# Kernel tuning notes

Measured on AMD Instinct MI355X. Metric: run time of the kernel, lower is better.

## Reference

```python
import jax, jax.numpy as jnp
import numpy as np

DIM = 32  # fixed internal node dim
N_GRAPHS = 64


def setup_inputs() -> dict:
    key = jax.random.key(0)
    ks = jax.random.split(key, 16)
    N, E, F_N, F_E, H = 12500, 200000, 16, 8, 32
    inp = {
        "x": jax.random.normal(ks[0], (N, F_N), dtype=jnp.float32),
        "edge_index": jax.random.randint(ks[1], (2, E), 0, N, dtype=jnp.int64),
        "edge_attr": jax.random.normal(ks[2], (E, F_E), dtype=jnp.float32),
        "batch": jnp.sort(jax.random.randint(ks[3], (N,), 0, N_GRAPHS, dtype=jnp.int64)),
        "lin0_w": jax.random.normal(ks[4], (DIM, F_N), dtype=jnp.float32) * 0.1,
        "lin0_b": jax.random.normal(ks[5], (DIM,), dtype=jnp.float32) * 0.1,
        "nn_w": jax.random.normal(ks[6], (DIM * H, F_E), dtype=jnp.float32) * 0.1,
        "nn_b": jax.random.normal(ks[7], (DIM * H,), dtype=jnp.float32) * 0.1,
        "root_w": jax.random.normal(ks[8], (DIM, H), dtype=jnp.float32) * 0.1,
        "conv_b": jax.random.normal(ks[9], (H,), dtype=jnp.float32) * 0.1,
        "lin1_w": jax.random.normal(ks[10], (16, H), dtype=jnp.float32) * 0.1,
        "lin1_b": jax.random.normal(ks[11], (16,), dtype=jnp.float32) * 0.1,
        "lin2_w": jax.random.normal(ks[12], (1, 16), dtype=jnp.float32) * 0.1,
        "lin2_b": jax.random.normal(ks[13], (1,), dtype=jnp.float32) * 0.1,
    }
    return inp


def reference(x, edge_index, edge_attr, batch, lin0_w, lin0_b, nn_w, nn_b,
              root_w, conv_b, lin1_w, lin1_b, lin2_w, lin2_b):
    N = x.shape[0]
    H = conv_b.shape[0]
    # lin0 + relu -> node features [N, DIM]
    out = jax.nn.relu(x @ lin0_w.T + lin0_b)
    # NNConv: per-edge weight matrices from edge MLP (single Linear)
    src, dst = edge_index[0], edge_index[1]
    w_e = (edge_attr @ nn_w.T + nn_b).reshape(-1, DIM, H)  # [E, DIM, H]
    msg = jnp.einsum('ed,edh->eh', out[src], w_e)          # gather + per-edge matmul
    agg = jax.ops.segment_sum(msg, dst, num_segments=N)     # scatter-add
    h = jax.nn.relu(agg + out @ root_w + conv_b)             # root weight + bias
    # global add pool over graphs
    u = jax.ops.segment_sum(h, batch, num_segments=N_GRAPHS)  # [G, H]
    o = jax.nn.relu(u @ lin1_w.T + lin1_b)
    o = o @ lin2_w.T + lin2_b
    return o.reshape(-1)
```

## Files before the change

kernel.cpp:

```cpp
#include <hip/hip_runtime.h>

#define DIMN 32
#define HD   32
#define FN   16
#define FE   8
#define NG   64
#define NPB1 16
#define NPB3 64

__global__ __launch_bounds__(256) void k1_node_pre(
    const float* __restrict__ x, const float* __restrict__ lin0_w,
    const float* __restrict__ lin0_b, const float* __restrict__ nn_w,
    const float* __restrict__ nn_b,
    float* __restrict__ outn, float* __restrict__ G, float* __restrict__ bmsg,
    float* __restrict__ agg, float* __restrict__ u, int N)
{
    __shared__ float s_nnw[DIMN * HD * FE];
    __shared__ float s_nnb[DIMN * HD];
    __shared__ float s_l0w[DIMN * FN];
    __shared__ float s_l0b[DIMN];
    __shared__ float s_out[NPB1 * DIMN];

    const int tid = threadIdx.x;
    for (int i = tid; i < DIMN * HD * FE; i += 256) s_nnw[i] = nn_w[i];
    for (int i = tid; i < DIMN * HD; i += 256)      s_nnb[i] = nn_b[i];
    for (int i = tid; i < DIMN * FN; i += 256)      s_l0w[i] = lin0_w[i];
    if (tid < DIMN) s_l0b[tid] = lin0_b[tid];

    const int n0 = blockIdx.x * NPB1;

    {
        const int a0 = n0 * HD;
        const int a1 = min((n0 + NPB1) * HD, N * HD);
        for (int i = a0 + tid; i < a1; i += 256) agg[i] = 0.f;
        if (blockIdx.x < (NG * HD) / 256) u[blockIdx.x * 256 + tid] = 0.f;
    }
    __syncthreads();

    #pragma unroll
    for (int pass = 0; pass < 2; ++pass) {
        const int nl = pass * 8 + (tid >> 5);
        const int d  = tid & 31;
        const int n  = n0 + nl;
        if (n < N) {
            float s = s_l0b[d];
            const float* xr = x + (size_t)n * FN;
            #pragma unroll
            for (int j = 0; j < FN; ++j) s = fmaf(xr[j], s_l0w[d * FN + j], s);
            s = fmaxf(s, 0.f);
            s_out[nl * DIMN + d] = s;
            outn[(size_t)n * DIMN + d] = s;
        }
    }
    __syncthreads();

    for (int nl = 0; nl < NPB1; ++nl) {
        const int n = n0 + nl;
        if (n >= N) break;
        float g = 0.f;
        #pragma unroll 8
        for (int d = 0; d < DIMN; ++d)
            g = fmaf(s_out[nl * DIMN + d], s_nnw[d * 256 + tid], g);
        G[(size_t)n * 256 + tid] = g;
    }

    #pragma unroll
    for (int pass = 0; pass < 2; ++pass) {
        const int nl = pass * 8 + (tid >> 5);
        const int h  = tid & 31;
        const int n  = n0 + nl;
        if (n < N) {
            float b = 0.f;
            #pragma unroll 8
            for (int d = 0; d < DIMN; ++d)
                b = fmaf(s_out[nl * DIMN + d], s_nnb[d * HD + h], b);
            bmsg[(size_t)n * HD + h] = b;
        }
    }
}

__global__ __launch_bounds__(256) void k2_edge(
    const int* __restrict__ ei, const float* __restrict__ ea,
    const float* __restrict__ G, const float* __restrict__ bmsg,
    float* __restrict__ agg, int E)
{
    const int t = blockIdx.x * 256 + threadIdx.x;
    const int e = t >> 5;
    const int h = t & 31;
    if (e >= E) return;

    const int src = ei[e];
    const int dst = ei[E + e];

    const float* gp = G + (size_t)src * 256 + h * 8;
    const float4 ga = *(const float4*)(gp);
    const float4 gb = *(const float4*)(gp + 4);
    const float4 e0 = *(const float4*)(ea + (size_t)e * 8);
    const float4 e1 = *(const float4*)(ea + (size_t)e * 8 + 4);

    float acc = bmsg[(size_t)src * HD + h];
    acc = fmaf(e0.x, ga.x, acc);
    acc = fmaf(e0.y, ga.y, acc);
    acc = fmaf(e0.z, ga.z, acc);
    acc = fmaf(e0.w, ga.w, acc);
    acc = fmaf(e1.x, gb.x, acc);
    acc = fmaf(e1.y, gb.y, acc);
    acc = fmaf(e1.z, gb.z, acc);
    acc = fmaf(e1.w, gb.w, acc);

    atomicAdd(agg + (size_t)dst * HD + h, acc);
}

__global__ __launch_bounds__(256) void k3_node_upd(
    const float* __restrict__ agg, const float* __restrict__ outn,
    const float* __restrict__ root_w, const float* __restrict__ conv_b,
    const int* __restrict__ batch, float* __restrict__ u, int N)
{
    __shared__ float s_rw[DIMN * HD];
    __shared__ float s_cb[HD];
    const int tid = threadIdx.x;
    for (int i = tid; i < DIMN * HD; i += 256) s_rw[i] = root_w[i];
    if (tid < HD) s_cb[tid] = conv_b[tid];
    __syncthreads();

    const int sg   = tid >> 5;
    const int h    = tid & 31;
    const int base = blockIdx.x * NPB3 + sg * (NPB3 / 8);

    float acc  = 0.f;
    int  g_cur = -1;
    #pragma unroll
    for (int i = 0; i < NPB3 / 8; ++i) {
        const int n = base + i;
        if (n >= N) break;

        float v = agg[(size_t)n * HD + h] + s_cb[h];
        const float* orow = outn + (size_t)n * DIMN;
        #pragma unroll 8
        for (int k = 0; k < DIMN; ++k)
            v = fmaf(orow[k], s_rw[k * HD + h], v);
        v = fmaxf(v, 0.f);

        const int g = (int)batch[n];
        if (g != g_cur) {
            if (g_cur >= 0) atomicAdd(u + (size_t)g_cur * HD + h, acc);
            g_cur = g;
            acc = v;
        } else {
            acc += v;
        }
    }
    if (g_cur >= 0) atomicAdd(u + (size_t)g_cur * HD + h, acc);
}

__global__ __launch_bounds__(64) void k4_head(
    const float* __restrict__ u, const float* __restrict__ lin1_w,
    const float* __restrict__ lin1_b, const float* __restrict__ lin2_w,
    const float* __restrict__ lin2_b, float* __restrict__ outp)
{
    const int g = threadIdx.x;
    if (g >= NG) return;

    float ur[HD];
    #pragma unroll
    for (int hh = 0; hh < HD; ++hh) ur[hh] = u[(size_t)g * HD + hh];

    float acc = lin2_b[0];
    #pragma unroll
    for (int i = 0; i < 16; ++i) {
        float o = lin1_b[i];
        #pragma unroll
        for (int hh = 0; hh < HD; ++hh)
            o = fmaf(ur[hh], lin1_w[i * HD + hh], o);
        o = fmaxf(o, 0.f);
        acc = fmaf(o, lin2_w[i], acc);
    }
    outp[g] = acc;
}

extern "C" void kernel_launch(void* const* d_in, const int* in_sizes, int n_in,
                              void* d_out, int out_size, void* d_ws, size_t ws_size,
                              hipStream_t stream)
{
    const float* x      = (const float*)d_in[0];
    const int*   ei     = (const int*)  d_in[1];
    const float* ea     = (const float*)d_in[2];
    const int*   batch  = (const int*)  d_in[3];
    const float* lin0_w = (const float*)d_in[4];
    const float* lin0_b = (const float*)d_in[5];
    const float* nn_w   = (const float*)d_in[6];
    const float* nn_b   = (const float*)d_in[7];
    const float* root_w = (const float*)d_in[8];
    const float* conv_b = (const float*)d_in[9];
    const float* lin1_w = (const float*)d_in[10];
    const float* lin1_b = (const float*)d_in[11];
    const float* lin2_w = (const float*)d_in[12];
    const float* lin2_b = (const float*)d_in[13];

    const int N = in_sizes[0] / FN;
    const int E = in_sizes[2] / FE;

    float* ws   = (float*)d_ws;
    float* outn = ws;
    float* G    = outn + (size_t)N * DIMN;
    float* bmsg = G    + (size_t)N * 256;
    float* agg  = bmsg + (size_t)N * DIMN;
    float* u    = agg  + (size_t)N * DIMN;

    const int nb1 = (N + NPB1 - 1) / NPB1;
    k1_node_pre<<<nb1, 256, 0, stream>>>(x, lin0_w, lin0_b, nn_w, nn_b,
                                         outn, G, bmsg, agg, u, N);

    const int nb2 = (E * 32 + 255) / 256;
    k2_edge<<<nb2, 256, 0, stream>>>(ei, ea, G, bmsg, agg, E);

    const int nb3 = (N + NPB3 - 1) / NPB3;
    k3_node_upd<<<nb3, 256, 0, stream>>>(agg, outn, root_w, conv_b, batch, u, N);

    k4_head<<<1, 64, 0, stream>>>(u, lin1_w, lin1_b, lin2_w, lin2_b, (float*)d_out);
}
```

Measured before the change: 157.9 us.

## Bucket edges by destination and gather messages per node instead of scatter atomics

Replaces the per-edge scatter kernel, which issued 32 float atomicAdds per edge into agg, with a bucketing pass. That pass does one integer atomic per edge to build fixed-capacity per-destination edge lists, with a slow per-edge fallback for nodes that overflow. A fused gather kernel then has one wavefront per group of nodes sum its incoming messages in registers, apply the root weight with shuffles, and pool into graphs. This removes most float atomic traffic and the separate node-update kernel, at the cost of an extra eidx buffer, an unsorted gather, and load imbalance on high-degree nodes.

Result: slower. 175.9 us (+11.4%).

```diff
diff --git a/kernel.cpp b/kernel.cpp
--- a/kernel.cpp
+++ b/kernel.cpp
@@ -6,14 +6,15 @@
 #define FE   8
 #define NG   64
 #define NPB1 16
-#define NPB3 64
+#define CAP  64
+#define NPW  4
 
 __global__ __launch_bounds__(256) void k1_node_pre(
     const float* __restrict__ x, const float* __restrict__ lin0_w,
     const float* __restrict__ lin0_b, const float* __restrict__ nn_w,
     const float* __restrict__ nn_b,
     float* __restrict__ outn, float* __restrict__ G, float* __restrict__ bmsg,
-    float* __restrict__ agg, float* __restrict__ u, int N)
+    float* __restrict__ agg, float* __restrict__ u, int* __restrict__ deg, int N)
 {
     __shared__ float s_nnw[DIMN * HD * FE];
     __shared__ float s_nnb[DIMN * HD];
@@ -33,6 +34,7 @@
         const int a0 = n0 * HD;
         const int a1 = min((n0 + NPB1) * HD, N * HD);
         for (int i = a0 + tid; i < a1; i += 256) agg[i] = 0.f;
+        if (tid < NPB1 && n0 + tid < N) deg[n0 + tid] = 0;
         if (blockIdx.x < (NG * HD) / 256) u[blockIdx.x * 256 + tid] = 0.f;
     }
     __syncthreads();
@@ -79,39 +81,33 @@
     }
 }
 
-__global__ __launch_bounds__(256) void k2_edge(
+__global__ __launch_bounds__(256) void kb_bucket(
     const int* __restrict__ ei, const float* __restrict__ ea,
     const float* __restrict__ G, const float* __restrict__ bmsg,
-    float* __restrict__ agg, int E)
-{
-    const int t = blockIdx.x * 256 + threadIdx.x;
-    const int e = t >> 5;
-    const int h = t & 31;
+    int* __restrict__ deg, int* __restrict__ eidx, float* __restrict__ agg, int E)
+{
+    const int e = blockIdx.x * 256 + threadIdx.x;
     if (e >= E) return;
-
-    const int src = ei[e];
     const int dst = ei[E + e];
-
-    const float* gp = G + (size_t)src * 256 + h * 8;
-    const float4 ga = *(const float4*)(gp);
-    const float4 gb = *(const float4*)(gp + 4);
-    const float4 e0 = *(const float4*)(ea + (size_t)e * 8);
-    const float4 e1 = *(const float4*)(ea + (size_t)e * 8 + 4);
-
-    float acc = bmsg[(size_t)src * HD + h];
-    acc = fmaf(e0.x, ga.x, acc);
-    acc = fmaf(e0.y, ga.y, acc);
-    acc = fmaf(e0.z, ga.z, acc);
-    acc = fmaf(e0.w, ga.w, acc);
-    acc = fmaf(e1.x, gb.x, acc);
-    acc = fmaf(e1.y, gb.y, acc);
-    acc = fmaf(e1.z, gb.z, acc);
-    acc = fmaf(e1.w, gb.w, acc);
-
-    atomicAdd(agg + (size_t)dst * HD + h, acc);
-}
-
-__global__ __launch_bounds__(256) void k3_node_upd(
+    const int pos = atomicAdd(&deg[dst], 1);
+    if (pos < CAP) {
+        eidx[dst * CAP + pos] = e;
+    } else {
+        const int src = ei[e];
+        for (int h = 0; h < HD; ++h) {
+            float m = bmsg[(size_t)src * HD + h];
+            #pragma unroll
+            for (int f = 0; f < FE; ++f)
+                m = fmaf(ea[(size_t)e * FE + f], G[(size_t)src * 256 + h * FE + f], m);
+            atomicAdd(agg + (size_t)dst * HD + h, m);
+        }
+    }
+}
+
+__global__ __launch_bounds__(256) void k23_gather_upd(
+    const int* __restrict__ ei, const float* __restrict__ ea,
+    const float* __restrict__ G, const float* __restrict__ bmsg,
+    const int* __restrict__ deg, const int* __restrict__ eidx,
     const float* __restrict__ agg, const float* __restrict__ outn,
     const float* __restrict__ root_w, const float* __restrict__ conv_b,
     const int* __restrict__ batch, float* __restrict__ u, int N)
@@ -123,34 +119,61 @@
     if (tid < HD) s_cb[tid] = conv_b[tid];
     __syncthreads();
 
-    const int sg   = tid >> 5;
-    const int h    = tid & 31;
-    const int base = blockIdx.x * NPB3 + sg * (NPB3 / 8);
-
-    float acc  = 0.f;
-    int  g_cur = -1;
-    #pragma unroll
-    for (int i = 0; i < NPB3 / 8; ++i) {
-        const int n = base + i;
+    const int lane  = tid & 63;
+    const int h     = lane & 31;
+    const int p     = lane >> 5;
+    const int wid   = (blockIdx.x * 256 + tid) >> 6;
+    const int nbase = wid * NPW;
+
+    float accp  = 0.f;
+    int   g_cur = -1;
+
+    for (int i = 0; i < NPW; ++i) {
+        const int n = nbase + i;
         if (n >= N) break;
 
-        float v = agg[(size_t)n * HD + h] + s_cb[h];
-        const float* orow = outn + (size_t)n * DIMN;
-        #pragma unroll 8
+        const int dn = min(deg[n], CAP);
+        float acc = 0.f;
+        for (int j = p; j < dn; j += 2) {
+            const int e   = eidx[n * CAP + j];
+            const int src = ei[e];
+            const float4 w0 = *(const float4*)(ea + (size_t)e * FE);
+            const float4 w1 = *(const float4*)(ea + (size_t)e * FE + 4);
+            const float* gp = G + (size_t)src * 256 + h * 8;
+            const float4 ga = *(const float4*)(gp);
+            const float4 gb = *(const float4*)(gp + 4);
+            float m = bmsg[(size_t)src * HD + h];
+            m = fmaf(w0.x, ga.x, m);
+            m = fmaf(w0.y, ga.y, m);
+            m = fmaf(w0.z, ga.z, m);
+            m = fmaf(w0.w, ga.w, m);
+            m = fmaf(w1.x, gb.x, m);
+            m = fmaf(w1.y, gb.y, m);
+            m = fmaf(w1.z, gb.z, m);
+            m = fmaf(w1.w, gb.w, m);
+            acc += m;
+        }
+        acc += __shfl_xor(acc, 32);
+
+        float v = acc + s_cb[h] + agg[(size_t)n * HD + h];
+        const float orow = outn[(size_t)n * DIMN + h];
+        #pragma unroll
         for (int k = 0; k < DIMN; ++k)
-            v = fmaf(orow[k], s_rw[k * HD + h], v);
+            v = fmaf(__shfl(orow, k, 32), s_rw[k * HD + h], v);
         v = fmaxf(v, 0.f);
 
-        const int g = (int)batch[n];
+        const int g = batch[n];
         if (g != g_cur) {
-            if (g_cur >= 0) atomicAdd(u + (size_t)g_cur * HD + h, acc);
+            if (g_cur >= 0 && p == 0)
+                atomicAdd(u + (size_t)g_cur * HD + h, accp);
             g_cur = g;
-            acc = v;
+            accp = v;
         } else {
-            acc += v;
-        }
-    }
-    if (g_cur >= 0) atomicAdd(u + (size_t)g_cur * HD + h, acc);
+            accp += v;
+        }
+    }
+    if (g_cur >= 0 && p == 0)
+        atomicAdd(u + (size_t)g_cur * HD + h, accp);
 }
 
 __global__ __launch_bounds__(64) void k4_head(
@@ -206,16 +229,20 @@
     float* bmsg = G    + (size_t)N * 256;
     float* agg  = bmsg + (size_t)N * DIMN;
     float* u    = agg  + (size_t)N * DIMN;
+    int*   deg  = (int*)(u + (size_t)NG * HD);
+    int*   eidx = deg + N;
 
     const int nb1 = (N + NPB1 - 1) / NPB1;
     k1_node_pre<<<nb1, 256, 0, stream>>>(x, lin0_w, lin0_b, nn_w, nn_b,
-                                         outn, G, bmsg, agg, u, N);
-
-    const int nb2 = (E * 32 + 255) / 256;
-    k2_edge<<<nb2, 256, 0, stream>>>(ei, ea, G, bmsg, agg, E);
-
-    const int nb3 = (N + NPB3 - 1) / NPB3;
-    k3_node_upd<<<nb3, 256, 0, stream>>>(agg, outn, root_w, conv_b, batch, u, N);
+                                         outn, G, bmsg, agg, u, deg, N);
+
+    const int nbb = (E + 255) / 256;
+    kb_bucket<<<nbb, 256, 0, stream>>>(ei, ea, G, bmsg, deg, eidx, agg, E);
+
+    const int nwaves = (N + NPW - 1) / NPW;
+    const int nb23   = (nwaves + 3) / 4;
+    k23_gather_upd<<<nb23, 256, 0, stream>>>(ei, ea, G, bmsg, deg, eidx, agg,
+                                             outn, root_w, conv_b, batch, u, N);
 
     k4_head<<<1, 64, 0, stream>>>(u, lin1_w, lin1_b, lin2_w, lin2_b, (float*)d_out);
 }
```
